# Performance work log

Hardware: AMD Instinct MI355X
Metric: run time of the kernel (lower is better)

Reference implementation:

```python
import jax, jax.numpy as jnp
import numpy as np

B, T, C, HS = 64, 256, 2048, 128


def setup_inputs() -> dict:
    key = jax.random.key(0)
    k1, k2, k3, k4 = jax.random.split(key, 4)
    x = jax.random.normal(k1, (B, T, C), dtype=jnp.float32)
    # Dense(head_size, use_bias=False) kernels, scaled like glorot-ish init
    Wk = jax.random.normal(k2, (C, HS), dtype=jnp.float32) * (C ** -0.5)
    Wq = jax.random.normal(k3, (C, HS), dtype=jnp.float32) * (C ** -0.5)
    Wv = jax.random.normal(k4, (C, HS), dtype=jnp.float32) * (C ** -0.5)
    return {"x": x, "Wk": Wk, "Wq": Wq, "Wv": Wv}


def reference(x, Wk, Wq, Wv):
    Bn, Tn, Cn = x.shape
    k = jnp.einsum("btc,ch->bth", x, Wk)
    q = jnp.einsum("btc,ch->bth", x, Wq)
    v = jnp.einsum("btc,ch->bth", x, Wv)
    # faithful to source: scores = k @ q^T, scaled by C**-0.5 (input dim!)
    scores = jnp.einsum("bth,bsh->bts", k, q) * (Cn ** -0.5)
    causal = jnp.tril(jnp.ones((Tn, Tn), dtype=bool))  # [T, T]
    scores = jnp.where(causal, scores, -jnp.inf)
    weights = jax.nn.softmax(scores, axis=-1)
    return jnp.einsum("bts,bsh->bth", weights, v)
```

## Files before the change

### kernel.cpp

```cpp
#include <hip/hip_runtime.h>
#include <hip/hip_bf16.h>
#include <cstdint>
#include <cstddef>

#define B_  64
#define T_  256
#define C_  2048
#define HS_ 128
#define N_  384

typedef __bf16 bf16x8 __attribute__((ext_vector_type(8)));
typedef float  floatx4 __attribute__((ext_vector_type(4)));

__device__ __forceinline__ unsigned short f2bf_rne(float f) {
  union { float f; unsigned int u; } v; v.f = f;
  unsigned int r = v.u + 0x7fffu + ((v.u >> 16) & 1u);
  return (unsigned short)(r >> 16);
}
__device__ __forceinline__ unsigned short f2bf(float f) {
  union { float f; unsigned int u; } v; v.f = f;
  return (unsigned short)((v.u + 0x8000u) >> 16);
}

__device__ __forceinline__ void async_copy16(const void* g, void* l) {
  __builtin_amdgcn_global_load_lds(
      (const __attribute__((address_space(1))) unsigned int*)g,
      (__attribute__((address_space(3))) unsigned int*)l, 16, 0, 0);
}

__global__ __launch_bounds__(256) void wt_kernel(
    const float* __restrict__ Wk, const float* __restrict__ Wq,
    const float* __restrict__ Wv, unsigned short* __restrict__ Wt) {
  __shared__ float tile[32][33];
  const int w  = blockIdx.z;
  const int c0 = blockIdx.x * 32;
  const int h0 = blockIdx.y * 32;
  const float* W = (w == 0) ? Wk : (w == 1) ? Wq : Wv;
  const int tx = threadIdx.x & 31, ty = threadIdx.x >> 5;
#pragma unroll
  for (int i = 0; i < 32; i += 8)
    tile[ty + i][tx] = W[(size_t)(c0 + ty + i) * HS_ + h0 + tx];
  __syncthreads();
#pragma unroll
  for (int i = 0; i < 32; i += 8) {
    int hh = ty + i, cc = tx;
    Wt[(size_t)(w * HS_ + h0 + hh) * C_ + c0 + cc] = f2bf_rne(tile[cc][hh]);
  }
}

__global__ __launch_bounds__(256) void qkv_gemm(
    const float* __restrict__ X, const unsigned short* __restrict__ Wt,
    unsigned short* __restrict__ kqv, unsigned short* __restrict__ vT) {
  __shared__ unsigned short As[2][64 * 72];
  __shared__ unsigned short Bs[2][128 * 64];

  const int tid  = threadIdx.x;
  const int wave = tid >> 6, lane = tid & 63;
  const int quad = lane >> 4, l16 = lane & 15;

  const int g  = blockIdx.x;
  const int ml = g & 7, q8 = g >> 3;
  const int nb = q8 % 3, mh = q8 / 3;
  const int m0 = (mh * 8 + ml) * 64;
  const int n0 = nb * 128;
  const int wm = (wave >> 1) * 32;
  const int wn = (wave & 1) * 64;

  const int arow = tid >> 4;
  const int achk = tid & 15;

  int bsrc_n[4], bsrc_c[4], bdst[4];
#pragma unroll
  for (int r = 0; r < 4; ++r) {
    int slot = (r * 4 + wave) * 64 + lane;
    int n = slot >> 3, sl = slot & 7;
    bsrc_n[r] = n; bsrc_c[r] = sl ^ (n & 7);
    bdst[r] = (r * 4 + wave) * 64 * 8;
  }

#pragma unroll
  for (int r = 0; r < 4; ++r)
    async_copy16(Wt + (size_t)(n0 + bsrc_n[r]) * C_ + bsrc_c[r] * 8,
                 &Bs[0][bdst[r]]);
  float4 av[4];
#pragma unroll
  for (int r = 0; r < 4; ++r)
    av[r] = *(const float4*)(X + (size_t)(m0 + arow + r * 16) * C_ + achk * 4);

  floatx4 acc[2][4] = {};

  for (int k = 0; k < 32; ++k) {
    const int cur = k & 1, nxt = cur ^ 1;
#pragma unroll
    for (int r = 0; r < 4; ++r) {
      ushort4 b4;
      b4.x = f2bf(av[r].x); b4.y = f2bf(av[r].y);
      b4.z = f2bf(av[r].z); b4.w = f2bf(av[r].w);
      *(ushort4*)&As[cur][(arow + r * 16) * 72 + achk * 4] = b4;
    }
    __syncthreads();

    if (k < 31) {
      const int kn = (k + 1) * 64;
#pragma unroll
      for (int r = 0; r < 4; ++r)
        async_copy16(Wt + (size_t)(n0 + bsrc_n[r]) * C_ + kn + bsrc_c[r] * 8,
                     &Bs[nxt][bdst[r]]);
#pragma unroll
      for (int r = 0; r < 4; ++r)
        av[r] = *(const float4*)(X + (size_t)(m0 + arow + r * 16) * C_ + kn + achk * 4);
    }

#pragma unroll
    for (int ks = 0; ks < 2; ++ks) {
      bf16x8 af[2], bfv[4];
#pragma unroll
      for (int mt = 0; mt < 2; ++mt)
        af[mt] = *(const bf16x8*)&As[cur][(wm + mt * 16 + l16) * 72 + ks * 32 + quad * 8];
#pragma unroll
      for (int nt = 0; nt < 4; ++nt) {
        int n = wn + nt * 16 + l16;
        int c = ks * 4 + quad;
        bfv[nt] = *(const bf16x8*)&Bs[cur][n * 64 + (c ^ (n & 7)) * 8];
      }
#pragma unroll
      for (int mt = 0; mt < 2; ++mt)
#pragma unroll
        for (int nt = 0; nt < 4; ++nt)
          acc[mt][nt] = __builtin_amdgcn_mfma_f32_16x16x32_bf16(
              af[mt], bfv[nt], acc[mt][nt], 0, 0, 0);
    }
  }

#pragma unroll
  for (int mt = 0; mt < 2; ++mt)
#pragma unroll
    for (int nt = 0; nt < 4; ++nt)
#pragma unroll
      for (int r = 0; r < 4; ++r) {
        int row = m0 + wm + mt * 16 + quad * 4 + r;
        int col = wn + nt * 16 + l16;
        unsigned short us = f2bf(acc[mt][nt][r]);
        kqv[(size_t)row * N_ + n0 + col] = us;
        if (n0 == 256) {
          int bb = row >> 8, tt = row & 255;
          vT[(size_t)bb * HS_ * T_ + (size_t)col * T_ + tt] = us;
        }
      }
}

__global__ __launch_bounds__(256) void attn_kernel(
    const unsigned short* __restrict__ kqv, const unsigned short* __restrict__ vT,
    float* __restrict__ out) {
  __shared__ unsigned short P[4][16 * 136];
  __shared__ float Olds[2][16][132];
  __shared__ float rs1[2][16];

  const int tid  = threadIdx.x;
  const int wave = tid >> 6, lane = tid & 63;
  const int quad = lane >> 4, l16 = lane & 15;
  const int tile = wave >> 1, par = wave & 1;
  const int tt = blockIdx.x * 2 + tile;
  const int b  = blockIdx.y;
  const int t0 = tt * 16;
  const float scale = 0.022097086912079612f;
  const unsigned short* kq = kqv + (size_t)b * T_ * N_;

  bf16x8 kf[4];
#pragma unroll
  for (int ks = 0; ks < 4; ++ks)
    kf[ks] = *(const bf16x8*)&kq[(size_t)(t0 + l16) * N_ + ks * 32 + quad * 8];

  const int n_my = ((tt + 1) + (1 - par)) >> 1;
  const int npad = (n_my + 1) & ~1;

  float rsum[4] = {0.f, 0.f, 0.f, 0.f};

  bf16x8 qf[4];
  if (n_my > 0) {
    const int st = par;
#pragma unroll
    for (int ks = 0; ks < 4; ++ks)
      qf[ks] = *(const bf16x8*)&kq[(size_t)(st * 16 + l16) * N_ + HS_ + ks * 32 + quad * 8];
  }
  for (int j = 0; j < n_my; ++j) {
    bf16x8 qn[4];
    if (j + 1 < n_my) {
      const int st = par + 2 * (j + 1);
#pragma unroll
      for (int ks = 0; ks < 4; ++ks)
        qn[ks] = *(const bf16x8*)&kq[(size_t)(st * 16 + l16) * N_ + HS_ + ks * 32 + quad * 8];
    }
    floatx4 a = {};
#pragma unroll
    for (int ks = 0; ks < 4; ++ks)
      a = __builtin_amdgcn_mfma_f32_16x16x32_bf16(kf[ks], qf[ks], a, 0, 0, 0);
    const int st = par + 2 * j;
    const int scol = st * 16 + l16;
#pragma unroll
    for (int r = 0; r < 4; ++r) {
      int trow = t0 + quad * 4 + r;
      float p = (scol <= trow) ? __expf(a[r] * scale) : 0.f;
      rsum[r] += p;
      P[wave][(quad * 4 + r) * 136 + j * 16 + l16] = f2bf(p);
    }
#pragma unroll
    for (int ks = 0; ks < 4; ++ks) qf[ks] = qn[ks];
  }
  if (npad > n_my) {
#pragma unroll
    for (int r = 0; r < 4; ++r)
      P[wave][(quad * 4 + r) * 136 + n_my * 16 + l16] = 0;
  }
#pragma unroll
  for (int m = 1; m < 16; m <<= 1)
#pragma unroll
    for (int r = 0; r < 4; ++r)
      rsum[r] += __shfl_xor(rsum[r], m, 64);

  floatx4 oacc[8] = {};
  const unsigned short* vb = vT + (size_t)b * HS_ * T_;
  const int nks = npad >> 1;
  const int sb_off = (quad >> 1);
  const int sb_lo  = (quad & 1) * 8;
  bf16x8 bv[8]; bf16x8 pa;
  if (nks > 0) {
    int st = par + 2 * (0 + sb_off);
    int sbase = st * 16 + sb_lo;
    pa = *(const bf16x8*)&P[wave][l16 * 136 + 0 * 32 + quad * 8];
#pragma unroll
    for (int nt = 0; nt < 8; ++nt)
      bv[nt] = *(const bf16x8*)&vb[(size_t)(nt * 16 + l16) * T_ + sbase];
  }
  for (int ks2 = 0; ks2 < nks; ++ks2) {
    bf16x8 bvn[8]; bf16x8 pan;
    if (ks2 + 1 < nks) {
      int jt = 2 * (ks2 + 1) + sb_off;
      int st = par + 2 * jt;
      int sbase = st * 16 + sb_lo;
      pan = *(const bf16x8*)&P[wave][l16 * 136 + (ks2 + 1) * 32 + quad * 8];
#pragma unroll
      for (int nt = 0; nt < 8; ++nt)
        bvn[nt] = *(const bf16x8*)&vb[(size_t)(nt * 16 + l16) * T_ + sbase];
    }
#pragma unroll
    for (int nt = 0; nt < 8; ++nt)
      oacc[nt] = __builtin_amdgcn_mfma_f32_16x16x32_bf16(pa, bv[nt], oacc[nt], 0, 0, 0);
    pa = pan;
#pragma unroll
    for (int nt = 0; nt < 8; ++nt) bv[nt] = bvn[nt];
  }

  if (par == 1) {
#pragma unroll
    for (int nt = 0; nt < 8; ++nt)
#pragma unroll
      for (int r = 0; r < 4; ++r)
        Olds[tile][quad * 4 + r][nt * 16 + l16] = oacc[nt][r];
    if (l16 == 0) {
#pragma unroll
      for (int r = 0; r < 4; ++r) rs1[tile][quad * 4 + r] = rsum[r];
    }
  }
  __syncthreads();
  if (par == 0) {
    float inv[4];
#pragma unroll
    for (int r = 0; r < 4; ++r)
      inv[r] = 1.f / (rsum[r] + rs1[tile][quad * 4 + r]);
    float* ob = out + ((size_t)b * T_ + t0) * HS_;
#pragma unroll
    for (int nt = 0; nt < 8; ++nt)
#pragma unroll
      for (int r = 0; r < 4; ++r) {
        int row = quad * 4 + r;
        ob[(size_t)row * HS_ + nt * 16 + l16] =
            (oacc[nt][r] + Olds[tile][row][nt * 16 + l16]) * inv[r];
      }
  }
}

extern "C" void kernel_launch(void* const* d_in, const int* in_sizes, int n_in,
                              void* d_out, int out_size, void* d_ws, size_t ws_size,
                              hipStream_t stream) {
  const float* x  = (const float*)d_in[0];
  const float* Wk = (const float*)d_in[1];
  const float* Wq = (const float*)d_in[2];
  const float* Wv = (const float*)d_in[3];
  float* out = (float*)d_out;

  char* ws = (char*)d_ws;
  unsigned short* Wt  = (unsigned short*)(ws);
  unsigned short* kqv = (unsigned short*)(ws + 1572864);
  unsigned short* vT  = (unsigned short*)(ws + 1572864 + 12582912);

  hipLaunchKernelGGL(wt_kernel, dim3(64, 4, 3), dim3(256), 0, stream, Wk, Wq, Wv, Wt);
  hipLaunchKernelGGL(qkv_gemm, dim3(768), dim3(256), 0, stream, x, Wt, kqv, vT);
  hipLaunchKernelGGL(attn_kernel, dim3(8, 64), dim3(256), 0, stream, kqv, vT, out);
}
```

Measured before the change: 244.4 us.

## Restructure QKV GEMM so each block computes all 384 columns, reading X once

The QKV projection GEMM now gives each 512-thread block a 64-row strip and the full 384-wide output (K, Q and V together), so each fp32 row of X is read from memory once instead of three times. X is loaded straight into registers in MFMA fragment layout and converted to bf16 there, which removes the A-tile staging through LDS. Only the weights go through LDS, in a 32-wide k-step double buffer. The catch is a grid of only 256 blocks, one wave of work on the device, plus twice as many barriers per k, and the B tile no longer uses the XOR swizzle, which may cause LDS bank conflicts.

```diff
diff --git a/kernel.cpp b/kernel.cpp
--- a/kernel.cpp
+++ b/kernel.cpp
@@ -26,6 +26,13 @@
   __builtin_amdgcn_global_load_lds(
       (const __attribute__((address_space(1))) unsigned int*)g,
       (__attribute__((address_space(3))) unsigned int*)l, 16, 0, 0);
+}
+
+__device__ __forceinline__ bf16x8 cvt8(const float4& a, const float4& b) {
+  union { unsigned short u[8]; bf16x8 v; } r;
+  r.u[0] = f2bf(a.x); r.u[1] = f2bf(a.y); r.u[2] = f2bf(a.z); r.u[3] = f2bf(a.w);
+  r.u[4] = f2bf(b.x); r.u[5] = f2bf(b.y); r.u[6] = f2bf(b.z); r.u[7] = f2bf(b.w);
+  return r.v;
 }
 
 __global__ __launch_bounds__(256) void wt_kernel(
@@ -48,105 +55,116 @@
   }
 }
 
-__global__ __launch_bounds__(256) void qkv_gemm(
+__global__ __launch_bounds__(512) void qkv_gemm(
     const float* __restrict__ X, const unsigned short* __restrict__ Wt,
     unsigned short* __restrict__ kqv, unsigned short* __restrict__ vT) {
-  __shared__ unsigned short As[2][64 * 72];
-  __shared__ unsigned short Bs[2][128 * 64];
+  __shared__ unsigned short Bs[2][N_ * 32];
 
   const int tid  = threadIdx.x;
   const int wave = tid >> 6, lane = tid & 63;
   const int quad = lane >> 4, l16 = lane & 15;
 
-  const int g  = blockIdx.x;
-  const int ml = g & 7, q8 = g >> 3;
-  const int nb = q8 % 3, mh = q8 / 3;
-  const int m0 = (mh * 8 + ml) * 64;
-  const int n0 = nb * 128;
-  const int wm = (wave >> 1) * 32;
-  const int wn = (wave & 1) * 64;
-
-  const int arow = tid >> 4;
-  const int achk = tid & 15;
-
-  int bsrc_n[4], bsrc_c[4], bdst[4];
-#pragma unroll
-  for (int r = 0; r < 4; ++r) {
-    int slot = (r * 4 + wave) * 64 + lane;
-    int n = slot >> 3, sl = slot & 7;
-    bsrc_n[r] = n; bsrc_c[r] = sl ^ (n & 7);
-    bdst[r] = (r * 4 + wave) * 64 * 8;
-  }
-
-#pragma unroll
-  for (int r = 0; r < 4; ++r)
-    async_copy16(Wt + (size_t)(n0 + bsrc_n[r]) * C_ + bsrc_c[r] * 8,
-                 &Bs[0][bdst[r]]);
-  float4 av[4];
-#pragma unroll
-  for (int r = 0; r < 4; ++r)
-    av[r] = *(const float4*)(X + (size_t)(m0 + arow + r * 16) * C_ + achk * 4);
-
-  floatx4 acc[2][4] = {};
-
-  for (int k = 0; k < 32; ++k) {
-    const int cur = k & 1, nxt = cur ^ 1;
-#pragma unroll
-    for (int r = 0; r < 4; ++r) {
-      ushort4 b4;
-      b4.x = f2bf(av[r].x); b4.y = f2bf(av[r].y);
-      b4.z = f2bf(av[r].z); b4.w = f2bf(av[r].w);
-      *(ushort4*)&As[cur][(arow + r * 16) * 72 + achk * 4] = b4;
-    }
-    __syncthreads();
-
-    if (k < 31) {
-      const int kn = (k + 1) * 64;
-#pragma unroll
-      for (int r = 0; r < 4; ++r)
-        async_copy16(Wt + (size_t)(n0 + bsrc_n[r]) * C_ + kn + bsrc_c[r] * 8,
-                     &Bs[nxt][bdst[r]]);
-#pragma unroll
-      for (int r = 0; r < 4; ++r)
-        av[r] = *(const float4*)(X + (size_t)(m0 + arow + r * 16) * C_ + kn + achk * 4);
-    }
-
-#pragma unroll
-    for (int ks = 0; ks < 2; ++ks) {
-      bf16x8 af[2], bfv[4];
-#pragma unroll
-      for (int mt = 0; mt < 2; ++mt)
-        af[mt] = *(const bf16x8*)&As[cur][(wm + mt * 16 + l16) * 72 + ks * 32 + quad * 8];
-#pragma unroll
-      for (int nt = 0; nt < 4; ++nt) {
-        int n = wn + nt * 16 + l16;
-        int c = ks * 4 + quad;
-        bfv[nt] = *(const bf16x8*)&Bs[cur][n * 64 + (c ^ (n & 7)) * 8];
-      }
-#pragma unroll
-      for (int mt = 0; mt < 2; ++mt)
-#pragma unroll
-        for (int nt = 0; nt < 4; ++nt)
-          acc[mt][nt] = __builtin_amdgcn_mfma_f32_16x16x32_bf16(
-              af[mt], bfv[nt], acc[mt][nt], 0, 0, 0);
+  const int m0 = blockIdx.x * 64;
+  const int wm = (wave >> 2) * 32;
+  const int wn = (wave & 3) * 96;
+
+  int dn[3], dc[3], ddst[3];
+#pragma unroll
+  for (int r = 0; r < 3; ++r) {
+    int s = r * 512 + tid;
+    dn[r]   = s >> 2;
+    dc[r]   = s & 3;
+    ddst[r] = (r * 512 + wave * 64) * 8;
+  }
+
+  const float* xr0 = X + (size_t)(m0 + wm + l16) * C_ + quad * 8;
+  const float* xr1 = xr0 + (size_t)16 * C_;
+
+#pragma unroll
+  for (int r = 0; r < 3; ++r)
+    async_copy16(Wt + (size_t)dn[r] * C_ + dc[r] * 8, &Bs[0][ddst[r]]);
+  float4 ava[4], avb[4];
+  ava[0] = *(const float4*)(xr0);
+  ava[1] = *(const float4*)(xr0 + 4);
+  ava[2] = *(const float4*)(xr1);
+  ava[3] = *(const float4*)(xr1 + 4);
+  avb[0] = *(const float4*)(xr0 + 32);
+  avb[1] = *(const float4*)(xr0 + 36);
+  avb[2] = *(const float4*)(xr1 + 32);
+  avb[3] = *(const float4*)(xr1 + 36);
+
+  floatx4 acc[2][6] = {};
+
+  for (int k = 0; k < 64; k += 2) {
+    {
+      bf16x8 af0 = cvt8(ava[0], ava[1]);
+      bf16x8 af1 = cvt8(ava[2], ava[3]);
+      __syncthreads();
+      {
+        const int kn = (k + 1) * 32;
+#pragma unroll
+        for (int r = 0; r < 3; ++r)
+          async_copy16(Wt + (size_t)dn[r] * C_ + kn + dc[r] * 8, &Bs[1][ddst[r]]);
+      }
+      if (k + 2 < 64) {
+        const int kn = (k + 2) * 32;
+        ava[0] = *(const float4*)(xr0 + kn);
+        ava[1] = *(const float4*)(xr0 + kn + 4);
+        ava[2] = *(const float4*)(xr1 + kn);
+        ava[3] = *(const float4*)(xr1 + kn + 4);
+      }
+#pragma unroll
+      for (int nt = 0; nt < 6; ++nt) {
+        const int n = wn + nt * 16 + l16;
+        bf16x8 bv = *(const bf16x8*)&Bs[0][n * 32 + quad * 8];
+        acc[0][nt] = __builtin_amdgcn_mfma_f32_16x16x32_bf16(af0, bv, acc[0][nt], 0, 0, 0);
+        acc[1][nt] = __builtin_amdgcn_mfma_f32_16x16x32_bf16(af1, bv, acc[1][nt], 0, 0, 0);
+      }
+    }
+    {
+      bf16x8 af0 = cvt8(avb[0], avb[1]);
+      bf16x8 af1 = cvt8(avb[2], avb[3]);
+      __syncthreads();
+      if (k + 2 < 64) {
+        const int kn = (k + 2) * 32;
+#pragma unroll
+        for (int r = 0; r < 3; ++r)
+          async_copy16(Wt + (size_t)dn[r] * C_ + kn + dc[r] * 8, &Bs[0][ddst[r]]);
+      }
+      if (k + 3 < 64) {
+        const int kn = (k + 3) * 32;
+        avb[0] = *(const float4*)(xr0 + kn);
+        avb[1] = *(const float4*)(xr0 + kn + 4);
+        avb[2] = *(const float4*)(xr1 + kn);
+        avb[3] = *(const float4*)(xr1 + kn + 4);
+      }
+#pragma unroll
+      for (int nt = 0; nt < 6; ++nt) {
+        const int n = wn + nt * 16 + l16;
+        bf16x8 bv = *(const bf16x8*)&Bs[1][n * 32 + quad * 8];
+        acc[0][nt] = __builtin_amdgcn_mfma_f32_16x16x32_bf16(af0, bv, acc[0][nt], 0, 0, 0);
+        acc[1][nt] = __builtin_amdgcn_mfma_f32_16x16x32_bf16(af1, bv, acc[1][nt], 0, 0, 0);
+      }
     }
   }
 
 #pragma unroll
   for (int mt = 0; mt < 2; ++mt)
 #pragma unroll
-    for (int nt = 0; nt < 4; ++nt)
+    for (int nt = 0; nt < 6; ++nt) {
+      const int colb = wn + nt * 16;
 #pragma unroll
       for (int r = 0; r < 4; ++r) {
         int row = m0 + wm + mt * 16 + quad * 4 + r;
-        int col = wn + nt * 16 + l16;
+        int col = colb + l16;
         unsigned short us = f2bf(acc[mt][nt][r]);
-        kqv[(size_t)row * N_ + n0 + col] = us;
-        if (n0 == 256) {
+        kqv[(size_t)row * N_ + col] = us;
+        if (colb >= 256) {
           int bb = row >> 8, tt = row & 255;
-          vT[(size_t)bb * HS_ * T_ + (size_t)col * T_ + tt] = us;
+          vT[(size_t)bb * HS_ * T_ + (size_t)(col - 256) * T_ + tt] = us;
         }
       }
+    }
 }
 
 __global__ __launch_bounds__(256) void attn_kernel(
@@ -295,6 +313,6 @@
   unsigned short* vT  = (unsigned short*)(ws + 1572864 + 12582912);
 
   hipLaunchKernelGGL(wt_kernel, dim3(64, 4, 3), dim3(256), 0, stream, Wk, Wq, Wv, Wt);
-  hipLaunchKernelGGL(qkv_gemm, dim3(768), dim3(256), 0, stream, x, Wt, kqv, vT);
+  hipLaunchKernelGGL(qkv_gemm, dim3(256), dim3(512), 0, stream, x, Wt, kqv, vT);
   hipLaunchKernelGGL(attn_kernel, dim3(8, 64), dim3(256), 0, stream, kqv, vT, out);
 }
```

Result: slower. 289.9 us (+18.6%).

## Load GEMM A operand straight into MFMA registers and balance causal attention tiles

Applied to the files above, without the earlier changes.

In the QKV GEMM, each lane now reads the fp32 rows of X it needs in MFMA fragment layout and converts them to bf16 in registers. This removes the LDS staging buffer for A, along with its shared-memory writes and reads. The cost is that waves sharing the same rows load them redundantly from global memory, and more registers hold the prefetched data. A launch-bounds occupancy hint of 3 blocks is added, and the attention kernel pairs query tile bx with tile 15-bx so each block gets a balanced amount of causal work.

```diff
diff --git a/kernel.cpp b/kernel.cpp
--- a/kernel.cpp
+++ b/kernel.cpp
@@ -26,6 +26,13 @@
   __builtin_amdgcn_global_load_lds(
       (const __attribute__((address_space(1))) unsigned int*)g,
       (__attribute__((address_space(3))) unsigned int*)l, 16, 0, 0);
+}
+
+__device__ __forceinline__ bf16x8 cvt8(const float4& a, const float4& b) {
+  union { unsigned short u[8]; bf16x8 v; } r;
+  r.u[0] = f2bf(a.x); r.u[1] = f2bf(a.y); r.u[2] = f2bf(a.z); r.u[3] = f2bf(a.w);
+  r.u[4] = f2bf(b.x); r.u[5] = f2bf(b.y); r.u[6] = f2bf(b.z); r.u[7] = f2bf(b.w);
+  return r.v;
 }
 
 __global__ __launch_bounds__(256) void wt_kernel(
@@ -48,10 +55,9 @@
   }
 }
 
-__global__ __launch_bounds__(256) void qkv_gemm(
+__global__ __launch_bounds__(256, 3) void qkv_gemm(
     const float* __restrict__ X, const unsigned short* __restrict__ Wt,
     unsigned short* __restrict__ kqv, unsigned short* __restrict__ vT) {
-  __shared__ unsigned short As[2][64 * 72];
   __shared__ unsigned short Bs[2][128 * 64];
 
   const int tid  = threadIdx.x;
@@ -66,9 +72,6 @@
   const int wm = (wave >> 1) * 32;
   const int wn = (wave & 1) * 64;
 
-  const int arow = tid >> 4;
-  const int achk = tid & 15;
-
   int bsrc_n[4], bsrc_c[4], bdst[4];
 #pragma unroll
   for (int r = 0; r < 4; ++r) {
@@ -78,26 +81,29 @@
     bdst[r] = (r * 4 + wave) * 64 * 8;
   }
 
+  const float* xr0 = X + (size_t)(m0 + wm + l16) * C_ + quad * 8;
+  const float* xr1 = xr0 + (size_t)16 * C_;
+
 #pragma unroll
   for (int r = 0; r < 4; ++r)
     async_copy16(Wt + (size_t)(n0 + bsrc_n[r]) * C_ + bsrc_c[r] * 8,
                  &Bs[0][bdst[r]]);
-  float4 av[4];
-#pragma unroll
-  for (int r = 0; r < 4; ++r)
-    av[r] = *(const float4*)(X + (size_t)(m0 + arow + r * 16) * C_ + achk * 4);
+  float4 av[8];
+  av[0] = *(const float4*)(xr0);       av[1] = *(const float4*)(xr0 + 4);
+  av[2] = *(const float4*)(xr0 + 32);  av[3] = *(const float4*)(xr0 + 36);
+  av[4] = *(const float4*)(xr1);       av[5] = *(const float4*)(xr1 + 4);
+  av[6] = *(const float4*)(xr1 + 32);  av[7] = *(const float4*)(xr1 + 36);
 
   floatx4 acc[2][4] = {};
 
   for (int k = 0; k < 32; ++k) {
     const int cur = k & 1, nxt = cur ^ 1;
-#pragma unroll
-    for (int r = 0; r < 4; ++r) {
-      ushort4 b4;
-      b4.x = f2bf(av[r].x); b4.y = f2bf(av[r].y);
-      b4.z = f2bf(av[r].z); b4.w = f2bf(av[r].w);
-      *(ushort4*)&As[cur][(arow + r * 16) * 72 + achk * 4] = b4;
-    }
+    bf16x8 af[2][2];
+    af[0][0] = cvt8(av[0], av[1]);
+    af[1][0] = cvt8(av[2], av[3]);
+    af[0][1] = cvt8(av[4], av[5]);
+    af[1][1] = cvt8(av[6], av[7]);
+
     __syncthreads();
 
     if (k < 31) {
@@ -106,17 +112,15 @@
       for (int r = 0; r < 4; ++r)
         async_copy16(Wt + (size_t)(n0 + bsrc_n[r]) * C_ + kn + bsrc_c[r] * 8,
                      &Bs[nxt][bdst[r]]);
-#pragma unroll
-      for (int r = 0; r < 4; ++r)
-        av[r] = *(const float4*)(X + (size_t)(m0 + arow + r * 16) * C_ + kn + achk * 4);
+      av[0] = *(const float4*)(xr0 + kn);       av[1] = *(const float4*)(xr0 + kn + 4);
+      av[2] = *(const float4*)(xr0 + kn + 32);  av[3] = *(const float4*)(xr0 + kn + 36);
+      av[4] = *(const float4*)(xr1 + kn);       av[5] = *(const float4*)(xr1 + kn + 4);
+      av[6] = *(const float4*)(xr1 + kn + 32);  av[7] = *(const float4*)(xr1 + kn + 36);
     }
 
 #pragma unroll
     for (int ks = 0; ks < 2; ++ks) {
-      bf16x8 af[2], bfv[4];
-#pragma unroll
-      for (int mt = 0; mt < 2; ++mt)
-        af[mt] = *(const bf16x8*)&As[cur][(wm + mt * 16 + l16) * 72 + ks * 32 + quad * 8];
+      bf16x8 bfv[4];
 #pragma unroll
       for (int nt = 0; nt < 4; ++nt) {
         int n = wn + nt * 16 + l16;
@@ -128,7 +132,7 @@
 #pragma unroll
         for (int nt = 0; nt < 4; ++nt)
           acc[mt][nt] = __builtin_amdgcn_mfma_f32_16x16x32_bf16(
-              af[mt], bfv[nt], acc[mt][nt], 0, 0, 0);
+              af[ks][mt], bfv[nt], acc[mt][nt], 0, 0, 0);
     }
   }
 
@@ -160,7 +164,7 @@
   const int wave = tid >> 6, lane = tid & 63;
   const int quad = lane >> 4, l16 = lane & 15;
   const int tile = wave >> 1, par = wave & 1;
-  const int tt = blockIdx.x * 2 + tile;
+  const int tt = tile ? (15 - (int)blockIdx.x) : (int)blockIdx.x;
   const int b  = blockIdx.y;
   const int t0 = tt * 16;
   const float scale = 0.022097086912079612f;
```

Result: slower. 282.8 us (+15.7%).

## Triple-buffer B tiles in QKV GEMM and balance causal tiles in attention

Applied to the files above, without the earlier changes.

The QKV GEMM moves to dynamic shared memory with a three-stage ring for the Wt tiles and two swizzled A buffers. B loads are issued two K-steps ahead, and manual waitcnt plus a raw s_barrier replace __syncthreads, so global loads overlap MFMA work. The A tile layout switches from padding to an XOR swizzle. The attention kernel now pairs query tile i with tile 15-i in each block, which evens out causal work across blocks. The hand-placed waitcnt and barrier scheme is fragile, and the larger shared memory footprint may reduce occupancy.

```diff
diff --git a/kernel.cpp b/kernel.cpp
--- a/kernel.cpp
+++ b/kernel.cpp
@@ -51,8 +51,7 @@
 __global__ __launch_bounds__(256) void qkv_gemm(
     const float* __restrict__ X, const unsigned short* __restrict__ Wt,
     unsigned short* __restrict__ kqv, unsigned short* __restrict__ vT) {
-  __shared__ unsigned short As[2][64 * 72];
-  __shared__ unsigned short Bs[2][128 * 64];
+  extern __shared__ char smem[];
 
   const int tid  = threadIdx.x;
   const int wave = tid >> 6, lane = tid & 63;
@@ -66,71 +65,105 @@
   const int wm = (wave >> 1) * 32;
   const int wn = (wave & 1) * 64;
 
-  const int arow = tid >> 4;
-  const int achk = tid & 15;
-
-  int bsrc_n[4], bsrc_c[4], bdst[4];
+  const unsigned short* bsrc[4]; int bdst[4];
 #pragma unroll
   for (int r = 0; r < 4; ++r) {
     int slot = (r * 4 + wave) * 64 + lane;
     int n = slot >> 3, sl = slot & 7;
-    bsrc_n[r] = n; bsrc_c[r] = sl ^ (n & 7);
-    bdst[r] = (r * 4 + wave) * 64 * 8;
-  }
-
-#pragma unroll
-  for (int r = 0; r < 4; ++r)
-    async_copy16(Wt + (size_t)(n0 + bsrc_n[r]) * C_ + bsrc_c[r] * 8,
-                 &Bs[0][bdst[r]]);
+    bsrc[r] = Wt + (size_t)(n0 + n) * C_ + (sl ^ (n & 7)) * 8;
+    bdst[r] = (r * 4 + wave) * 1024;
+  }
+  int arow[4], achk[4], awoff[4];
+#pragma unroll
+  for (int r = 0; r < 4; ++r) {
+    int s = r * 256 + tid;
+    arow[r] = s >> 4; achk[r] = s & 15;
+    awoff[r] = arow[r] * 128 + (((achk[r] >> 1) ^ (arow[r] & 7)) << 4) + ((achk[r] & 1) << 3);
+  }
+
+#define ISSUE_B(KT, OFF)                                                       \
+  {                                                                            \
+    _Pragma("unroll")                                                          \
+    for (int r = 0; r < 4; ++r)                                                \
+      async_copy16(bsrc[r] + (size_t)(KT) * 64, smem + (OFF) + bdst[r]);       \
+  }
+#define LOAD_A(KT)                                                             \
+  {                                                                            \
+    _Pragma("unroll")                                                          \
+    for (int r = 0; r < 4; ++r)                                                \
+      av[r] = *(const float4*)(X + (size_t)(m0 + arow[r]) * C_ + (KT) * 64 + achk[r] * 4); \
+  }
+#define STORE_A(BUF)                                                           \
+  {                                                                            \
+    _Pragma("unroll")                                                          \
+    for (int r = 0; r < 4; ++r) {                                              \
+      ushort4 b4;                                                              \
+      b4.x = f2bf(av[r].x); b4.y = f2bf(av[r].y);                              \
+      b4.z = f2bf(av[r].z); b4.w = f2bf(av[r].w);                              \
+      *(ushort4*)(smem + 49152 + (BUF) * 8192 + awoff[r]) = b4;                \
+    }                                                                          \
+  }
+
+  floatx4 acc[2][4] = {};
+
+#define COMPUTE(CUR, OFF)                                                      \
+  {                                                                            \
+    const char* ab = smem + 49152 + (CUR) * 8192;                              \
+    const char* bb = smem + (OFF);                                             \
+    _Pragma("unroll")                                                          \
+    for (int ks = 0; ks < 2; ++ks) {                                           \
+      bf16x8 af[2], bfv[4];                                                    \
+      _Pragma("unroll")                                                        \
+      for (int mt = 0; mt < 2; ++mt) {                                         \
+        int rr = wm + mt * 16 + l16;                                           \
+        af[mt] = *(const bf16x8*)(ab + rr * 128 + (((ks * 4 + quad) ^ (rr & 7)) << 4)); \
+      }                                                                        \
+      _Pragma("unroll")                                                        \
+      for (int nt = 0; nt < 4; ++nt) {                                         \
+        int n = wn + nt * 16 + l16;                                            \
+        bfv[nt] = *(const bf16x8*)(bb + n * 128 + (((ks * 4 + quad) ^ (n & 7)) << 4)); \
+      }                                                                        \
+      _Pragma("unroll")                                                        \
+      for (int mt = 0; mt < 2; ++mt)                                           \
+        _Pragma("unroll")                                                      \
+        for (int nt = 0; nt < 4; ++nt)                                         \
+          acc[mt][nt] = __builtin_amdgcn_mfma_f32_16x16x32_bf16(               \
+              af[mt], bfv[nt], acc[mt][nt], 0, 0, 0);                          \
+    }                                                                          \
+  }
+
   float4 av[4];
-#pragma unroll
-  for (int r = 0; r < 4; ++r)
-    av[r] = *(const float4*)(X + (size_t)(m0 + arow + r * 16) * C_ + achk * 4);
-
-  floatx4 acc[2][4] = {};
+  LOAD_A(0);
+  ISSUE_B(0, 0);
+  ISSUE_B(1, 16384);
+  asm volatile("s_waitcnt vmcnt(8)" ::: "memory");
+  STORE_A(0);
+  LOAD_A(1);
+  asm volatile("s_waitcnt vmcnt(8)" ::: "memory");
+  asm volatile("s_waitcnt lgkmcnt(0)" ::: "memory");
+
+  int off0 = 0, off1 = 16384, off2 = 32768;
 
   for (int k = 0; k < 32; ++k) {
     const int cur = k & 1, nxt = cur ^ 1;
-#pragma unroll
-    for (int r = 0; r < 4; ++r) {
-      ushort4 b4;
-      b4.x = f2bf(av[r].x); b4.y = f2bf(av[r].y);
-      b4.z = f2bf(av[r].z); b4.w = f2bf(av[r].w);
-      *(ushort4*)&As[cur][(arow + r * 16) * 72 + achk * 4] = b4;
-    }
-    __syncthreads();
-
+    __builtin_amdgcn_s_barrier();
+    __builtin_amdgcn_sched_barrier(0);
+    const int kt = (k + 2 < 32) ? (k + 2) : 31;
+    ISSUE_B(kt, off2);
+    COMPUTE(cur, off0);
+    asm volatile("s_waitcnt vmcnt(4)" ::: "memory");
     if (k < 31) {
-      const int kn = (k + 1) * 64;
-#pragma unroll
-      for (int r = 0; r < 4; ++r)
-        async_copy16(Wt + (size_t)(n0 + bsrc_n[r]) * C_ + kn + bsrc_c[r] * 8,
-                     &Bs[nxt][bdst[r]]);
-#pragma unroll
-      for (int r = 0; r < 4; ++r)
-        av[r] = *(const float4*)(X + (size_t)(m0 + arow + r * 16) * C_ + kn + achk * 4);
-    }
-
-#pragma unroll
-    for (int ks = 0; ks < 2; ++ks) {
-      bf16x8 af[2], bfv[4];
-#pragma unroll
-      for (int mt = 0; mt < 2; ++mt)
-        af[mt] = *(const bf16x8*)&As[cur][(wm + mt * 16 + l16) * 72 + ks * 32 + quad * 8];
-#pragma unroll
-      for (int nt = 0; nt < 4; ++nt) {
-        int n = wn + nt * 16 + l16;
-        int c = ks * 4 + quad;
-        bfv[nt] = *(const bf16x8*)&Bs[cur][n * 64 + (c ^ (n & 7)) * 8];
-      }
-#pragma unroll
-      for (int mt = 0; mt < 2; ++mt)
-#pragma unroll
-        for (int nt = 0; nt < 4; ++nt)
-          acc[mt][nt] = __builtin_amdgcn_mfma_f32_16x16x32_bf16(
-              af[mt], bfv[nt], acc[mt][nt], 0, 0, 0);
-    }
-  }
+      STORE_A(nxt);
+      if (k < 30) LOAD_A(k + 2);
+      asm volatile("s_waitcnt lgkmcnt(0)" ::: "memory");
+    }
+    int t = off0; off0 = off1; off1 = off2; off2 = t;
+  }
+  asm volatile("s_waitcnt vmcnt(0)" ::: "memory");
+#undef ISSUE_B
+#undef LOAD_A
+#undef STORE_A
+#undef COMPUTE
 
 #pragma unroll
   for (int mt = 0; mt < 2; ++mt)
@@ -160,7 +193,7 @@
   const int wave = tid >> 6, lane = tid & 63;
   const int quad = lane >> 4, l16 = lane & 15;
   const int tile = wave >> 1, par = wave & 1;
-  const int tt = blockIdx.x * 2 + tile;
+  const int tt = tile ? (15 - (int)blockIdx.x) : (int)blockIdx.x;
   const int b  = blockIdx.y;
   const int t0 = tt * 16;
   const float scale = 0.022097086912079612f;
@@ -294,7 +327,15 @@
   unsigned short* kqv = (unsigned short*)(ws + 1572864);
   unsigned short* vT  = (unsigned short*)(ws + 1572864 + 12582912);
 
+  static bool attr_set = false;
+  if (!attr_set) {
+    (void)hipFuncSetAttribute(reinterpret_cast<const void*>(qkv_gemm),
+                              hipFuncAttributeMaxDynamicSharedMemorySize,
+                              65536);
+    attr_set = true;
+  }
+
   hipLaunchKernelGGL(wt_kernel, dim3(64, 4, 3), dim3(256), 0, stream, Wk, Wq, Wv, Wt);
-  hipLaunchKernelGGL(qkv_gemm, dim3(768), dim3(256), 0, stream, x, Wt, kqv, vT);
+  hipLaunchKernelGGL(qkv_gemm, dim3(768), dim3(256), 65536, stream, x, Wt, kqv, vT);
   hipLaunchKernelGGL(attn_kernel, dim3(8, 64), dim3(256), 0, stream, kqv, vT, out);
 }
```

Result: slower. 259.6 us (+6.2%).
